# Optimization experiments

Hardware: AMD Instinct MI355X
Metric: run time of the kernel (lower is better)

The kernel has to match this reference:

```python
import jax, jax.numpy as jnp
import numpy as np

INPUT_DIM = 512
HIDDEN_DIM = 1024
OUTPUT_DIM = 1000
BATCH = 256
SEQ_LEN = 256


def setup_inputs() -> dict:
    key = jax.random.key(0)
    ks = jax.random.split(key, 7)
    std = 1.0 / np.sqrt(HIDDEN_DIM)
    u = lambda k, shape: jax.random.uniform(k, shape, jnp.float32, -std, std)
    return {
        "x": jax.random.normal(ks[0], (BATCH, SEQ_LEN, INPUT_DIM), jnp.float32),
        "w_x2h": u(ks[1], (4 * HIDDEN_DIM, INPUT_DIM)),
        "b_x2h": u(ks[2], (4 * HIDDEN_DIM,)),
        "w_h2h": u(ks[3], (4 * HIDDEN_DIM, HIDDEN_DIM)),
        "b_h2h": u(ks[4], (4 * HIDDEN_DIM,)),
        "w_fc": u(ks[5], (OUTPUT_DIM, HIDDEN_DIM)),
        "b_fc": u(ks[6], (OUTPUT_DIM,)),
    }


def _lstm_last_hidden(x, w_x2h, b_x2h, w_h2h, b_h2h):
    B, T, D = x.shape
    H = w_h2h.shape[1]
    # Precompute input-to-hidden for all timesteps in one big GEMM: [B,T,4H]
    xg = jnp.einsum("btd,gd->btg", x, w_x2h) + b_x2h + b_h2h
    xg = jnp.swapaxes(xg, 0, 1)  # [T,B,4H] for scan

    def step(carry, xg_t):
        h, c = carry
        gates = xg_t + h @ w_h2h.T  # [B,4H]
        i, f, g, o = jnp.split(gates, 4, axis=1)
        i = jax.nn.sigmoid(i)
        f = jax.nn.sigmoid(f)
        g = jnp.tanh(g)
        o = jax.nn.sigmoid(o)
        c = c * f + i * g
        h = o * jnp.tanh(c)
        return (h, c), None

    h0 = jnp.zeros((B, H), x.dtype)
    c0 = jnp.zeros((B, H), x.dtype)
    (h_last, _), _ = jax.lax.scan(step, (h0, c0), xg)
    return h_last


def reference(x, w_x2h, b_x2h, w_h2h, b_h2h, w_fc, b_fc):
    h_last = _lstm_last_hidden(x, w_x2h, b_x2h, w_h2h, b_h2h)  # [B,H]
    return h_last @ w_fc.T + b_fc  # [B,OUTPUT_DIM]
```

## Files before the change

kernel.cpp:

```cpp
#include <hip/hip_runtime.h>

typedef __attribute__((ext_vector_type(8))) short short8;
typedef __attribute__((ext_vector_type(4))) float floatx4;

#define DIN  512
#define HSZ  1024
#define G4   4096
#define KTOT 1536
#define BQ   256
#define TT   256

#define MFMA __builtin_amdgcn_mfma_f32_16x16x32_bf16

__device__ __forceinline__ unsigned short f2bf(float f){
  unsigned int u = __float_as_uint(f);
  u += 0x7fffu + ((u >> 16) & 1u);
  return (unsigned short)(u >> 16);
}
__device__ __forceinline__ unsigned int pack2(float a, float b){
  return (unsigned int)f2bf(a) | ((unsigned int)f2bf(b) << 16);
}

__global__ void prep_wcat(const float* __restrict__ wx, const float* __restrict__ wh,
                          const float* __restrict__ bx, const float* __restrict__ bh,
                          unsigned short* __restrict__ Wcat, float* __restrict__ bias){
  int gid = blockIdx.x * blockDim.x + threadIdx.x;
  int idx = gid * 8;
  int g = idx / KTOT;
  int k = idx - g * KTOT;
  const float* src = (k < DIN) ? (wx + (size_t)g * DIN + k)
                               : (wh + (size_t)g * HSZ + (k - DIN));
  float4 f0 = *(const float4*)(src);
  float4 f1 = *(const float4*)(src + 4);
  uint4 v = make_uint4(pack2(f0.x,f0.y), pack2(f0.z,f0.w), pack2(f1.x,f1.y), pack2(f1.z,f1.w));
  *(uint4*)(Wcat + (size_t)g * KTOT + k) = v;
  if (gid < G4) bias[gid] = bx[gid] + bh[gid];
}

__global__ void prep_wfc(const float* __restrict__ wfc, unsigned short* __restrict__ Wfcb){
  int gid = blockIdx.x * blockDim.x + threadIdx.x;
  int idx = gid * 8;
  int n = idx >> 10;
  int k = idx & 1023;
  uint4 v;
  if (n < 1000){
    const float* src = wfc + (size_t)n * 1024 + k;
    float4 f0 = *(const float4*)(src);
    float4 f1 = *(const float4*)(src + 4);
    v = make_uint4(pack2(f0.x,f0.y), pack2(f0.z,f0.w), pack2(f1.x,f1.y), pack2(f1.z,f1.w));
  } else {
    v = make_uint4(0u, 0u, 0u, 0u);
  }
  *(uint4*)(Wfcb + idx) = v;
}

__global__ void prep_x(const float* __restrict__ x, unsigned short* __restrict__ xbf){
  int gid = blockIdx.x * 256 + threadIdx.x;
  int d8 = gid & 63;
  int b  = (gid >> 6) & 255;
  int t  = gid >> 14;
  const float* src = x + (((size_t)b * TT) + t) * DIN + d8 * 8;
  float4 f0 = *(const float4*)(src);
  float4 f1 = *(const float4*)(src + 4);
  uint4 v = make_uint4(pack2(f0.x,f0.y), pack2(f0.z,f0.w), pack2(f1.x,f1.y), pack2(f1.z,f1.w));
  *(uint4*)(xbf + (((size_t)t * BQ) + b) * DIN + d8 * 8) = v;
}

__global__ void init_misc(unsigned int* __restrict__ h0w, unsigned int* __restrict__ flags, int nflags){
  int gid = blockIdx.x * 256 + threadIdx.x;
  if (gid < 131072) h0w[gid] = 0u;
  if (gid < nflags) flags[gid] = 0u;
}

__global__ __launch_bounds__(512, 2)
void lstm_persist(const unsigned short* __restrict__ xbf,
                  const unsigned short* __restrict__ Wcat,
                  const float* __restrict__ bias,
                  unsigned short* __restrict__ hseq,
                  unsigned int* __restrict__ leafcnt,
                  unsigned int* __restrict__ rootcnt,
                  unsigned int* __restrict__ done){
  extern __shared__ char smem[];
  char*  Ws  = smem;
  float* Gt  = (float*)(smem + 98304);
  float* Bls = (float*)(smem + 98304 + 16896);

  const int tid  = threadIdx.x;
  const int bx   = blockIdx.x;
  const int bg   = bx >> 7;
  const int hb   = bx & 127;
  const int b0   = bg << 7;
  const int u0   = hb << 3;
  const int lane = tid & 63;
  const int rg   = tid >> 6;

  {
    int c  = tid >> 4;
    int ch = tid & 15;
    int g  = c >> 3, j = c & 7;
    const char* src = (const char*)(Wcat + (size_t)(g * HSZ + u0 + j) * KTOT);
    char* dst = Ws + c * 3072;
    int xr = j << 4;
    #pragma unroll
    for (int q = 0; q < 12; ++q){
      int k2 = ch * 192 + q * 16;
      *(uint4*)(dst + (k2 ^ xr)) = *(const uint4*)(src + k2);
    }
    if (tid < 32) Bls[tid] = bias[(size_t)(tid >> 3) * HSZ + u0 + (tid & 7)];
  }
  __syncthreads();

  const int arow = lane & 15;
  const int kq8  = (lane >> 4) * 8;
  const int cc0  = lane & 15;
  const int cc1  = 16 + (lane & 15);
  const char* bp0 = Ws + cc0 * 3072; const int xr0 = (cc0 & 7) << 4;
  const char* bp1 = Ws + cc1 * 3072; const int xr1 = (cc1 & 7) << 4;

  const int erow = tid >> 2;
  const int eup  = (tid & 3) * 2;
  float cst0 = 0.f, cst1 = 0.f;

  const size_t growbase = (size_t)(b0 + rg * 16 + arow);

  for (int t = 0; t < TT; ++t){
    const unsigned short* hin  = hseq + (size_t)t * (BQ * HSZ);
    unsigned short*       hout = hseq + (size_t)(t + 1) * (BQ * HSZ);

    floatx4 acc[4][2];
    #pragma unroll
    for (int s = 0; s < 4; ++s){
      acc[s][0] = (floatx4){0.f,0.f,0.f,0.f};
      acc[s][1] = (floatx4){0.f,0.f,0.f,0.f};
    }

    {
      const unsigned short* xrow = xbf + ((size_t)t * BQ + growbase) * DIN + kq8;
      short8 av[4]; short8 bv[4][2];
      #pragma unroll
      for (int p = 0; p < 4; ++p){
        int k = p * 32;
        av[p]    = *(const short8*)(xrow + k);
        bv[p][0] = *(const short8*)(bp0 + ((2 * (k + kq8)) ^ xr0));
        bv[p][1] = *(const short8*)(bp1 + ((2 * (k + kq8)) ^ xr1));
      }
      #pragma unroll
      for (int ks = 0; ks < 16; ++ks){
        int sl = ks & 3;
        acc[sl][0] = MFMA(av[sl], bv[sl][0], acc[sl][0], 0, 0, 0);
        acc[sl][1] = MFMA(av[sl], bv[sl][1], acc[sl][1], 0, 0, 0);
        if (ks < 12){
          int k = (ks + 4) * 32;
          av[sl]    = *(const short8*)(xrow + k);
          bv[sl][0] = *(const short8*)(bp0 + ((2 * (k + kq8)) ^ xr0));
          bv[sl][1] = *(const short8*)(bp1 + ((2 * (k + kq8)) ^ xr1));
        }
      }
    }

    if (t > 0){
      if (tid == 0){
        const unsigned int* dp = &done[(((size_t)t * 2 + bg) * 16 + (hb & 15)) * 16];
        while (__hip_atomic_load(dp, __ATOMIC_RELAXED, __HIP_MEMORY_SCOPE_AGENT) == 0u)
          __builtin_amdgcn_s_sleep(2);
      }
      __syncthreads();
      asm volatile("" ::: "memory");
    }

    {
      const unsigned short* hrow = hin + growbase * HSZ + kq8;
      short8 ah[8]; short8 bh[8][2];
      #pragma unroll
      for (int p = 0; p < 8; ++p){
        int k = p * 32;
        ah[p] = *(const short8*)(hrow + k);
        int kb = 1024 + 2 * (k + kq8);
        bh[p][0] = *(const short8*)(bp0 + (kb ^ xr0));
        bh[p][1] = *(const short8*)(bp1 + (kb ^ xr1));
      }
      #pragma unroll
      for (int ks = 0; ks < 32; ++ks){
        int sl = ks & 7, as = ks & 3;
        acc[as][0] = MFMA(ah[sl], bh[sl][0], acc[as][0], 0, 0, 0);
        acc[as][1] = MFMA(ah[sl], bh[sl][1], acc[as][1], 0, 0, 0);
        if (ks < 24){
          int k = (ks + 8) * 32;
          ah[sl] = *(const short8*)(hrow + k);
          int kb = 1024 + 2 * (k + kq8);
          bh[sl][0] = *(const short8*)(bp0 + (kb ^ xr0));
          bh[sl][1] = *(const short8*)(bp1 + (kb ^ xr1));
        }
      }
    }

    floatx4 g0 = acc[0][0] + acc[1][0] + acc[2][0] + acc[3][0];
    floatx4 g1 = acc[0][1] + acc[1][1] + acc[2][1] + acc[3][1];

    {
      int r0 = rg * 16 + (lane >> 4) * 4;
      #pragma unroll
      for (int r = 0; r < 4; ++r){
        Gt[(r0 + r) * 33 + cc0] = g0[r];
        Gt[(r0 + r) * 33 + cc1] = g1[r];
      }
    }
    __syncthreads();

    {
      float cn0, cn1;
      {
        float gi = Gt[erow * 33 +      eup] + Bls[     eup];
        float gf = Gt[erow * 33 +  8 + eup] + Bls[ 8 + eup];
        float gg = Gt[erow * 33 + 16 + eup] + Bls[16 + eup];
        float go = Gt[erow * 33 + 24 + eup] + Bls[24 + eup];
        float iv = 1.f / (1.f + __expf(-gi));
        float fv = 1.f / (1.f + __expf(-gf));
        float e2 = __expf(-2.f * fmaxf(fminf(gg, 30.f), -30.f));
        float gv = (1.f - e2) / (1.f + e2);
        float ov = 1.f / (1.f + __expf(-go));
        cn0 = cst0 * fv + iv * gv;
        cst0 = cn0;
      }
      {
        float gi = Gt[erow * 33 +      eup + 1] + Bls[     eup + 1];
        float gf = Gt[erow * 33 +  8 + eup + 1] + Bls[ 8 + eup + 1];
        float gg = Gt[erow * 33 + 16 + eup + 1] + Bls[16 + eup + 1];
        float go = Gt[erow * 33 + 24 + eup + 1] + Bls[24 + eup + 1];
        float iv = 1.f / (1.f + __expf(-gi));
        float fv = 1.f / (1.f + __expf(-gf));
        float e2 = __expf(-2.f * fmaxf(fminf(gg, 30.f), -30.f));
        float gv = (1.f - e2) / (1.f + e2);
        float ov = 1.f / (1.f + __expf(-go));
        cn1 = cst1 * fv + iv * gv;
        cst1 = cn1;
        float e2c0 = __expf(-2.f * fmaxf(fminf(cn0, 30.f), -30.f));
        float h0v  = (1.f - e2c0) / (1.f + e2c0);
        float e2c1 = __expf(-2.f * fmaxf(fminf(cn1, 30.f), -30.f));
        float h1v  = (1.f - e2c1) / (1.f + e2c1);
        float go0 = Gt[erow * 33 + 24 + eup] + Bls[24 + eup];
        float ov0 = 1.f / (1.f + __expf(-go0));
        unsigned int packed = pack2(ov0 * h0v, ov * h1v);
        __hip_atomic_store((unsigned int*)(hout + (size_t)(b0 + erow) * HSZ + u0 + eup),
                           packed, __ATOMIC_RELAXED, __HIP_MEMORY_SCOPE_AGENT);
      }
    }
    __syncthreads();

    if (tid == 0){
      unsigned int old = __hip_atomic_fetch_add(
          &leafcnt[(((size_t)(t + 1) * 2 + bg) * 8 + (hb >> 4)) * 16], 1u,
          __ATOMIC_RELAXED, __HIP_MEMORY_SCOPE_AGENT);
      if (old == 15u){
        unsigned int old2 = __hip_atomic_fetch_add(
            &rootcnt[((size_t)(t + 1) * 2 + bg) * 16], 1u,
            __ATOMIC_RELAXED, __HIP_MEMORY_SCOPE_AGENT);
        if (old2 == 7u){
          #pragma unroll
          for (int cpy = 0; cpy < 16; ++cpy)
            __hip_atomic_store(&done[(((size_t)(t + 1) * 2 + bg) * 16 + cpy) * 16], 1u,
                               __ATOMIC_RELAXED, __HIP_MEMORY_SCOPE_AGENT);
        }
      }
    }
  }
}

__global__ __launch_bounds__(256, 1)
void fc_kernel(const unsigned short* __restrict__ h, const unsigned short* __restrict__ wfc,
               const float* __restrict__ bfc, float* __restrict__ out){
  int bx = blockIdx.x, tid = threadIdx.x;
  int wave = tid >> 6, lane = tid & 63;
  int row0 = (bx >> 4) * 64 + wave * 16;
  int col0 = (bx & 15) * 64;
  int lr = lane & 15, lk = (lane >> 4) * 8;
  floatx4 acc[4] = {{0.f,0.f,0.f,0.f},{0.f,0.f,0.f,0.f},{0.f,0.f,0.f,0.f},{0.f,0.f,0.f,0.f}};
  #pragma unroll 4
  for (int ks = 0; ks < 32; ++ks){
    int k = ks * 32 + lk;
    short8 a = *(const short8*)(h + (size_t)(row0 + lr) * 1024 + k);
    #pragma unroll
    for (int fj = 0; fj < 4; ++fj){
      short8 b = *(const short8*)(wfc + (size_t)(col0 + fj * 16 + lr) * 1024 + k);
      acc[fj] = MFMA(a, b, acc[fj], 0, 0, 0);
    }
  }
  #pragma unroll
  for (int fj = 0; fj < 4; ++fj){
    int col = col0 + fj * 16 + lr;
    if (col < 1000){
      #pragma unroll
      for (int r = 0; r < 4; ++r){
        int row = row0 + (lane >> 4) * 4 + r;
        out[(size_t)row * 1000 + col] = acc[fj][r] + bfc[col];
      }
    }
  }
}

extern "C" void kernel_launch(void* const* d_in, const int* in_sizes, int n_in,
                              void* d_out, int out_size, void* d_ws, size_t ws_size,
                              hipStream_t stream){
  const float* x    = (const float*)d_in[0];
  const float* wx2h = (const float*)d_in[1];
  const float* bx2h = (const float*)d_in[2];
  const float* wh2h = (const float*)d_in[3];
  const float* bh2h = (const float*)d_in[4];
  const float* wfc  = (const float*)d_in[5];
  const float* bfc  = (const float*)d_in[6];
  float* out = (float*)d_out;
  char* ws = (char*)d_ws;

  unsigned short* Wcat = (unsigned short*)(ws + 0);
  unsigned short* Wfcb = (unsigned short*)(ws + 12582912);
  float*          bias = (float*)         (ws + 14680064);
  unsigned short* xbf  = (unsigned short*)(ws + 14696448);
  unsigned short* hseq = (unsigned short*)(ws + 81805312);
  unsigned int*   leaf = (unsigned int*)  (ws + 216547328);
  unsigned int*   root = (unsigned int*)  (ws + 216810496);
  unsigned int*   done = (unsigned int*)  (ws + 216843392);

  (void)hipFuncSetAttribute((const void*)lstm_persist,
                            hipFuncAttributeMaxDynamicSharedMemorySize, 115456);

  hipLaunchKernelGGL(prep_wcat, dim3(3072), dim3(256), 0, stream, wx2h, wh2h, bx2h, bh2h, Wcat, bias);
  hipLaunchKernelGGL(prep_wfc,  dim3(512),  dim3(256), 0, stream, wfc, Wfcb);
  hipLaunchKernelGGL(prep_x,    dim3(16384),dim3(256), 0, stream, x, xbf);
  hipLaunchKernelGGL(init_misc, dim3(1318), dim3(256), 0, stream,
                     (unsigned int*)hseq, leaf, (int)((263168 + 32896 + 1052672) / 4));

  hipLaunchKernelGGL(lstm_persist, dim3(256), dim3(512), 115456, stream,
                     xbf, Wcat, bias, hseq, leaf, root, done);

  hipLaunchKernelGGL(fc_kernel, dim3(64), dim3(256), 0, stream,
                     hseq + (size_t)256 * BQ * HSZ, Wfcb, bfc, out);
}
```

Before: 3.182 ms.

## Split K across wave pairs with 32-row tiles and flat counter barrier

Each wave now computes a 32x32 tile (two row fragments by two column fragments) over half of the K range, with the two K-halves reduced through a doubled shared-memory gate buffer. The goal is more MFMA work per loaded A/B fragment and less LDS traffic for weights. The hierarchical leaf/root/done barrier is replaced with a single per-timestep counter that every block increments and polls until it reaches 128, with a shorter sleep. This gives a simpler, lower-latency sync in exchange for more atomic contention on one address and higher shared-memory use.

```diff
diff --git a/kernel.cpp b/kernel.cpp
--- a/kernel.cpp
+++ b/kernel.cpp
@@ -66,10 +66,10 @@
   *(uint4*)(xbf + (((size_t)t * BQ) + b) * DIN + d8 * 8) = v;
 }
 
-__global__ void init_misc(unsigned int* __restrict__ h0w, unsigned int* __restrict__ flags, int nflags){
+__global__ void init_misc(unsigned int* __restrict__ h0w, unsigned int* __restrict__ cnt, int ncnt){
   int gid = blockIdx.x * 256 + threadIdx.x;
   if (gid < 131072) h0w[gid] = 0u;
-  if (gid < nflags) flags[gid] = 0u;
+  if (gid < ncnt)   cnt[gid] = 0u;
 }
 
 __global__ __launch_bounds__(512, 2)
@@ -77,22 +77,21 @@
                   const unsigned short* __restrict__ Wcat,
                   const float* __restrict__ bias,
                   unsigned short* __restrict__ hseq,
-                  unsigned int* __restrict__ leafcnt,
-                  unsigned int* __restrict__ rootcnt,
-                  unsigned int* __restrict__ done){
+                  unsigned int* __restrict__ cnt){
   extern __shared__ char smem[];
   char*  Ws  = smem;
-  float* Gt  = (float*)(smem + 98304);
-  float* Bls = (float*)(smem + 98304 + 16896);
+  float* Gt2 = (float*)(smem + 98304);
+  float* Bls = (float*)(smem + 98304 + 34816);
 
   const int tid  = threadIdx.x;
   const int bx   = blockIdx.x;
   const int bg   = bx >> 7;
-  const int hb   = bx & 127;
   const int b0   = bg << 7;
-  const int u0   = hb << 3;
+  const int u0   = (bx & 127) << 3;
   const int lane = tid & 63;
-  const int rg   = tid >> 6;
+  const int w    = tid >> 6;
+  const int rg   = w & 3;
+  const int kg   = w >> 2;
 
   {
     int c  = tid >> 4;
@@ -110,158 +109,159 @@
   }
   __syncthreads();
 
-  const int arow = lane & 15;
   const int kq8  = (lane >> 4) * 8;
-  const int cc0  = lane & 15;
-  const int cc1  = 16 + (lane & 15);
-  const char* bp0 = Ws + cc0 * 3072; const int xr0 = (cc0 & 7) << 4;
-  const char* bp1 = Ws + cc1 * 3072; const int xr1 = (cc1 & 7) << 4;
+  const int cA   = lane & 15;
+  const int cB   = 16 + (lane & 15);
+  const char* bpA = Ws + cA * 3072; const int xorA = (cA & 7) << 4;
+  const char* bpB = Ws + cB * 3072; const int xorB = (cB & 7) << 4;
+
+  const size_t rowA0 = (size_t)(b0 + rg * 32 + (lane & 15));
 
   const int erow = tid >> 2;
   const int eup  = (tid & 3) * 2;
   float cst0 = 0.f, cst1 = 0.f;
 
-  const size_t growbase = (size_t)(b0 + rg * 16 + arow);
-
   for (int t = 0; t < TT; ++t){
     const unsigned short* hin  = hseq + (size_t)t * (BQ * HSZ);
     unsigned short*       hout = hseq + (size_t)(t + 1) * (BQ * HSZ);
 
-    floatx4 acc[4][2];
+    floatx4 acc[2][2][2];
     #pragma unroll
-    for (int s = 0; s < 4; ++s){
-      acc[s][0] = (floatx4){0.f,0.f,0.f,0.f};
-      acc[s][1] = (floatx4){0.f,0.f,0.f,0.f};
-    }
+    for (int ab = 0; ab < 2; ++ab)
+      #pragma unroll
+      for (int rf = 0; rf < 2; ++rf)
+        #pragma unroll
+        for (int cf = 0; cf < 2; ++cf)
+          acc[ab][rf][cf] = (floatx4){0.f,0.f,0.f,0.f};
 
     {
-      const unsigned short* xrow = xbf + ((size_t)t * BQ + growbase) * DIN + kq8;
-      short8 av[4]; short8 bv[4][2];
+      const unsigned short* xr0 = xbf + ((size_t)t * BQ + rowA0) * DIN + kg * 256 + kq8;
+      const unsigned short* xr1 = xr0 + (size_t)16 * DIN;
+      const int bbase = kg * 512 + kq8 * 2;
+      short8 a[4][2], b[4][2];
       #pragma unroll
       for (int p = 0; p < 4; ++p){
-        int k = p * 32;
-        av[p]    = *(const short8*)(xrow + k);
-        bv[p][0] = *(const short8*)(bp0 + ((2 * (k + kq8)) ^ xr0));
-        bv[p][1] = *(const short8*)(bp1 + ((2 * (k + kq8)) ^ xr1));
-      }
-      #pragma unroll
-      for (int ks = 0; ks < 16; ++ks){
-        int sl = ks & 3;
-        acc[sl][0] = MFMA(av[sl], bv[sl][0], acc[sl][0], 0, 0, 0);
-        acc[sl][1] = MFMA(av[sl], bv[sl][1], acc[sl][1], 0, 0, 0);
-        if (ks < 12){
-          int k = (ks + 4) * 32;
-          av[sl]    = *(const short8*)(xrow + k);
-          bv[sl][0] = *(const short8*)(bp0 + ((2 * (k + kq8)) ^ xr0));
-          bv[sl][1] = *(const short8*)(bp1 + ((2 * (k + kq8)) ^ xr1));
+        a[p][0] = *(const short8*)(xr0 + p * 32);
+        a[p][1] = *(const short8*)(xr1 + p * 32);
+        int bb = bbase + p * 64;
+        b[p][0] = *(const short8*)(bpA + (bb ^ xorA));
+        b[p][1] = *(const short8*)(bpB + (bb ^ xorB));
+      }
+      #pragma unroll
+      for (int j = 0; j < 8; ++j){
+        int sl = j & 3, ab = j & 1;
+        acc[ab][0][0] = MFMA(a[sl][0], b[sl][0], acc[ab][0][0], 0, 0, 0);
+        acc[ab][0][1] = MFMA(a[sl][0], b[sl][1], acc[ab][0][1], 0, 0, 0);
+        acc[ab][1][0] = MFMA(a[sl][1], b[sl][0], acc[ab][1][0], 0, 0, 0);
+        acc[ab][1][1] = MFMA(a[sl][1], b[sl][1], acc[ab][1][1], 0, 0, 0);
+        if (j < 4){
+          int jj = j + 4;
+          a[sl][0] = *(const short8*)(xr0 + jj * 32);
+          a[sl][1] = *(const short8*)(xr1 + jj * 32);
+          int bb = bbase + jj * 64;
+          b[sl][0] = *(const short8*)(bpA + (bb ^ xorA));
+          b[sl][1] = *(const short8*)(bpB + (bb ^ xorB));
         }
       }
     }
 
     if (t > 0){
       if (tid == 0){
-        const unsigned int* dp = &done[(((size_t)t * 2 + bg) * 16 + (hb & 15)) * 16];
-        while (__hip_atomic_load(dp, __ATOMIC_RELAXED, __HIP_MEMORY_SCOPE_AGENT) == 0u)
-          __builtin_amdgcn_s_sleep(2);
+        const unsigned int* cp = &cnt[((size_t)t * 2 + bg) * 32];
+        while (__hip_atomic_load(cp, __ATOMIC_RELAXED, __HIP_MEMORY_SCOPE_AGENT) < 128u)
+          __builtin_amdgcn_s_sleep(1);
       }
       __syncthreads();
       asm volatile("" ::: "memory");
     }
 
     {
-      const unsigned short* hrow = hin + growbase * HSZ + kq8;
-      short8 ah[8]; short8 bh[8][2];
-      #pragma unroll
-      for (int p = 0; p < 8; ++p){
-        int k = p * 32;
-        ah[p] = *(const short8*)(hrow + k);
-        int kb = 1024 + 2 * (k + kq8);
-        bh[p][0] = *(const short8*)(bp0 + (kb ^ xr0));
-        bh[p][1] = *(const short8*)(bp1 + (kb ^ xr1));
-      }
-      #pragma unroll
-      for (int ks = 0; ks < 32; ++ks){
-        int sl = ks & 7, as = ks & 3;
-        acc[as][0] = MFMA(ah[sl], bh[sl][0], acc[as][0], 0, 0, 0);
-        acc[as][1] = MFMA(ah[sl], bh[sl][1], acc[as][1], 0, 0, 0);
-        if (ks < 24){
-          int k = (ks + 8) * 32;
-          ah[sl] = *(const short8*)(hrow + k);
-          int kb = 1024 + 2 * (k + kq8);
-          bh[sl][0] = *(const short8*)(bp0 + (kb ^ xr0));
-          bh[sl][1] = *(const short8*)(bp1 + (kb ^ xr1));
+      const unsigned short* hr0 = hin + rowA0 * HSZ + kg * 512 + kq8;
+      const unsigned short* hr1 = hr0 + (size_t)16 * HSZ;
+      const int bbase = 1024 + kg * 1024 + kq8 * 2;
+      short8 a[4][2], b[4][2];
+      #pragma unroll
+      for (int p = 0; p < 4; ++p){
+        a[p][0] = *(const short8*)(hr0 + p * 32);
+        a[p][1] = *(const short8*)(hr1 + p * 32);
+        int bb = bbase + p * 64;
+        b[p][0] = *(const short8*)(bpA + (bb ^ xorA));
+        b[p][1] = *(const short8*)(bpB + (bb ^ xorB));
+      }
+      #pragma unroll
+      for (int j = 0; j < 16; ++j){
+        int sl = j & 3, ab = j & 1;
+        acc[ab][0][0] = MFMA(a[sl][0], b[sl][0], acc[ab][0][0], 0, 0, 0);
+        acc[ab][0][1] = MFMA(a[sl][0], b[sl][1], acc[ab][0][1], 0, 0, 0);
+        acc[ab][1][0] = MFMA(a[sl][1], b[sl][0], acc[ab][1][0], 0, 0, 0);
+        acc[ab][1][1] = MFMA(a[sl][1], b[sl][1], acc[ab][1][1], 0, 0, 0);
+        if (j < 12){
+          int jj = j + 4;
+          a[sl][0] = *(const short8*)(hr0 + jj * 32);
+          a[sl][1] = *(const short8*)(hr1 + jj * 32);
+          int bb = bbase + jj * 64;
+          b[sl][0] = *(const short8*)(bpA + (bb ^ xorA));
+          b[sl][1] = *(const short8*)(bpB + (bb ^ xorB));
         }
       }
     }
 
-    floatx4 g0 = acc[0][0] + acc[1][0] + acc[2][0] + acc[3][0];
-    floatx4 g1 = acc[0][1] + acc[1][1] + acc[2][1] + acc[3][1];
-
     {
-      int r0 = rg * 16 + (lane >> 4) * 4;
-      #pragma unroll
-      for (int r = 0; r < 4; ++r){
-        Gt[(r0 + r) * 33 + cc0] = g0[r];
-        Gt[(r0 + r) * 33 + cc1] = g1[r];
+      float* gdst = Gt2 + kg * (128 * 34);
+      int r0 = rg * 32 + (lane >> 4) * 4;
+      #pragma unroll
+      for (int rf = 0; rf < 2; ++rf){
+        floatx4 g0 = acc[0][rf][0] + acc[1][rf][0];
+        floatx4 g1 = acc[0][rf][1] + acc[1][rf][1];
+        #pragma unroll
+        for (int r = 0; r < 4; ++r){
+          gdst[(r0 + rf * 16 + r) * 34 + cA] = g0[r];
+          gdst[(r0 + rf * 16 + r) * 34 + cB] = g1[r];
+        }
       }
     }
     __syncthreads();
 
     {
-      float cn0, cn1;
-      {
-        float gi = Gt[erow * 33 +      eup] + Bls[     eup];
-        float gf = Gt[erow * 33 +  8 + eup] + Bls[ 8 + eup];
-        float gg = Gt[erow * 33 + 16 + eup] + Bls[16 + eup];
-        float go = Gt[erow * 33 + 24 + eup] + Bls[24 + eup];
-        float iv = 1.f / (1.f + __expf(-gi));
-        float fv = 1.f / (1.f + __expf(-gf));
-        float e2 = __expf(-2.f * fmaxf(fminf(gg, 30.f), -30.f));
-        float gv = (1.f - e2) / (1.f + e2);
-        float ov = 1.f / (1.f + __expf(-go));
-        cn0 = cst0 * fv + iv * gv;
-        cst0 = cn0;
-      }
-      {
-        float gi = Gt[erow * 33 +      eup + 1] + Bls[     eup + 1];
-        float gf = Gt[erow * 33 +  8 + eup + 1] + Bls[ 8 + eup + 1];
-        float gg = Gt[erow * 33 + 16 + eup + 1] + Bls[16 + eup + 1];
-        float go = Gt[erow * 33 + 24 + eup + 1] + Bls[24 + eup + 1];
-        float iv = 1.f / (1.f + __expf(-gi));
-        float fv = 1.f / (1.f + __expf(-gf));
-        float e2 = __expf(-2.f * fmaxf(fminf(gg, 30.f), -30.f));
-        float gv = (1.f - e2) / (1.f + e2);
-        float ov = 1.f / (1.f + __expf(-go));
-        cn1 = cst1 * fv + iv * gv;
-        cst1 = cn1;
-        float e2c0 = __expf(-2.f * fmaxf(fminf(cn0, 30.f), -30.f));
-        float h0v  = (1.f - e2c0) / (1.f + e2c0);
-        float e2c1 = __expf(-2.f * fmaxf(fminf(cn1, 30.f), -30.f));
-        float h1v  = (1.f - e2c1) / (1.f + e2c1);
-        float go0 = Gt[erow * 33 + 24 + eup] + Bls[24 + eup];
-        float ov0 = 1.f / (1.f + __expf(-go0));
-        unsigned int packed = pack2(ov0 * h0v, ov * h1v);
-        __hip_atomic_store((unsigned int*)(hout + (size_t)(b0 + erow) * HSZ + u0 + eup),
-                           packed, __ATOMIC_RELAXED, __HIP_MEMORY_SCOPE_AGENT);
-      }
+      const float* g0p = Gt2 + erow * 34;
+      const float* g1p = g0p + 128 * 34;
+      float gi0 = g0p[     eup] + g1p[     eup] + Bls[     eup];
+      float gf0 = g0p[ 8 + eup] + g1p[ 8 + eup] + Bls[ 8 + eup];
+      float gg0 = g0p[16 + eup] + g1p[16 + eup] + Bls[16 + eup];
+      float go0 = g0p[24 + eup] + g1p[24 + eup] + Bls[24 + eup];
+      float gi1 = g0p[     eup + 1] + g1p[     eup + 1] + Bls[     eup + 1];
+      float gf1 = g0p[ 8 + eup + 1] + g1p[ 8 + eup + 1] + Bls[ 8 + eup + 1];
+      float gg1 = g0p[16 + eup + 1] + g1p[16 + eup + 1] + Bls[16 + eup + 1];
+      float go1 = g0p[24 + eup + 1] + g1p[24 + eup + 1] + Bls[24 + eup + 1];
+
+      float iv0 = 1.f / (1.f + __expf(-gi0));
+      float fv0 = 1.f / (1.f + __expf(-gf0));
+      float e20 = __expf(-2.f * fmaxf(fminf(gg0, 30.f), -30.f));
+      float gv0 = (1.f - e20) / (1.f + e20);
+      float ov0 = 1.f / (1.f + __expf(-go0));
+      float cn0 = cst0 * fv0 + iv0 * gv0;
+      cst0 = cn0;
+      float ec0 = __expf(-2.f * fmaxf(fminf(cn0, 30.f), -30.f));
+      float hv0 = ov0 * (1.f - ec0) / (1.f + ec0);
+
+      float iv1 = 1.f / (1.f + __expf(-gi1));
+      float fv1 = 1.f / (1.f + __expf(-gf1));
+      float e21 = __expf(-2.f * fmaxf(fminf(gg1, 30.f), -30.f));
+      float gv1 = (1.f - e21) / (1.f + e21);
+      float ov1 = 1.f / (1.f + __expf(-go1));
+      float cn1 = cst1 * fv1 + iv1 * gv1;
+      cst1 = cn1;
+      float ec1 = __expf(-2.f * fmaxf(fminf(cn1, 30.f), -30.f));
+      float hv1 = ov1 * (1.f - ec1) / (1.f + ec1);
+
+      __hip_atomic_store((unsigned int*)(hout + (size_t)(b0 + erow) * HSZ + u0 + eup),
+                         pack2(hv0, hv1), __ATOMIC_RELAXED, __HIP_MEMORY_SCOPE_AGENT);
     }
     __syncthreads();
 
     if (tid == 0){
-      unsigned int old = __hip_atomic_fetch_add(
-          &leafcnt[(((size_t)(t + 1) * 2 + bg) * 8 + (hb >> 4)) * 16], 1u,
-          __ATOMIC_RELAXED, __HIP_MEMORY_SCOPE_AGENT);
-      if (old == 15u){
-        unsigned int old2 = __hip_atomic_fetch_add(
-            &rootcnt[((size_t)(t + 1) * 2 + bg) * 16], 1u,
-            __ATOMIC_RELAXED, __HIP_MEMORY_SCOPE_AGENT);
-        if (old2 == 7u){
-          #pragma unroll
-          for (int cpy = 0; cpy < 16; ++cpy)
-            __hip_atomic_store(&done[(((size_t)(t + 1) * 2 + bg) * 16 + cpy) * 16], 1u,
-                               __ATOMIC_RELAXED, __HIP_MEMORY_SCOPE_AGENT);
-        }
-      }
+      __hip_atomic_fetch_add(&cnt[((size_t)(t + 1) * 2 + bg) * 32], 1u,
+                             __ATOMIC_RELAXED, __HIP_MEMORY_SCOPE_AGENT);
     }
   }
 }
@@ -316,21 +316,19 @@
   float*          bias = (float*)         (ws + 14680064);
   unsigned short* xbf  = (unsigned short*)(ws + 14696448);
   unsigned short* hseq = (unsigned short*)(ws + 81805312);
-  unsigned int*   leaf = (unsigned int*)  (ws + 216547328);
-  unsigned int*   root = (unsigned int*)  (ws + 216810496);
-  unsigned int*   done = (unsigned int*)  (ws + 216843392);
+  unsigned int*   cntb = (unsigned int*)  (ws + 216547328);
 
   (void)hipFuncSetAttribute((const void*)lstm_persist,
-                            hipFuncAttributeMaxDynamicSharedMemorySize, 115456);
+                            hipFuncAttributeMaxDynamicSharedMemorySize, 133376);
 
   hipLaunchKernelGGL(prep_wcat, dim3(3072), dim3(256), 0, stream, wx2h, wh2h, bx2h, bh2h, Wcat, bias);
   hipLaunchKernelGGL(prep_wfc,  dim3(512),  dim3(256), 0, stream, wfc, Wfcb);
   hipLaunchKernelGGL(prep_x,    dim3(16384),dim3(256), 0, stream, x, xbf);
-  hipLaunchKernelGGL(init_misc, dim3(1318), dim3(256), 0, stream,
-                     (unsigned int*)hseq, leaf, (int)((263168 + 32896 + 1052672) / 4));
-
-  hipLaunchKernelGGL(lstm_persist, dim3(256), dim3(512), 115456, stream,
-                     xbf, Wcat, bias, hseq, leaf, root, done);
+  hipLaunchKernelGGL(init_misc, dim3(512),  dim3(256), 0, stream,
+                     (unsigned int*)hseq, cntb, (int)(65792 / 4));
+
+  hipLaunchKernelGGL(lstm_persist, dim3(256), dim3(512), 133376, stream,
+                     xbf, Wcat, bias, hseq, cntb);
 
   hipLaunchKernelGGL(fc_kernel, dim3(64), dim3(256), 0, stream,
                      hseq + (size_t)256 * BQ * HSZ, Wfcb, bfc, out);
```

Result: slower. 3.262 ms (+2.5%).
